# Optimization experiments

Measured on AMD Instinct MI355X. Metric: run time of the kernel, lower is better.

Reference implementation:

```python
import jax, jax.numpy as jnp
import numpy as np

N_NODES = 100000
N_EDGES = 1600000
D = 128


def setup_inputs() -> dict:
    key = jax.random.key(0)
    k1, k2, k3 = jax.random.split(key, 3)
    x = jax.random.normal(k1, (N_NODES, D), dtype=jnp.float32)
    edge_index = jax.random.randint(k2, (2, N_EDGES), 0, N_NODES, dtype=jnp.int64)
    weight = jax.random.normal(k3, (D, D), dtype=jnp.float32) * (1.0 / np.sqrt(D))
    bias = jnp.zeros((D,), dtype=jnp.float32)
    return {"x": x, "edge_index": edge_index, "weight": weight, "bias": bias}


def reference(x, edge_index, weight, bias):
    # Eval-mode forward: dropout(p=0.5, training=False) is identity.
    N = x.shape[0]
    row, col = edge_index[0], edge_index[1]  # source -> target

    # gcn_norm: add self loops (weight 1), symmetric normalization
    loop = jnp.arange(N, dtype=edge_index.dtype)
    full_row = jnp.concatenate([row, loop])
    full_col = jnp.concatenate([col, loop])
    ew = jnp.ones(full_row.shape[0], dtype=x.dtype)
    deg = jax.ops.segment_sum(ew, full_col, num_segments=N)
    deg_inv_sqrt = jnp.where(deg > 0, jax.lax.rsqrt(jnp.maximum(deg, 1e-12)), 0.0)
    norm = deg_inv_sqrt[full_row] * ew * deg_inv_sqrt[full_col]  # [E+N]

    # linear transform then gather-scale-scatter aggregation
    h = x @ weight.T  # [N, D]
    msgs = h[full_row] * norm[:, None]  # [E+N, D]
    out = jax.ops.segment_sum(msgs, full_col, num_segments=N)
    out = out + bias
    return jax.nn.relu(out)
```

## Files before the change

kernel.cpp:

```cpp
#include <hip/hip_runtime.h>

#define N_NODES 100000
#define N_EDGES 1600000
#define D 128
#define N_STRIPS (N_NODES / 32)

#define BSH   9
#define NBKT  196
#define P_BLK 160
#define EPB   (N_EDGES / P_BLK)

typedef __bf16 bf16x2 __attribute__((ext_vector_type(2)));
typedef __bf16 bf16x4 __attribute__((ext_vector_type(4)));
typedef __bf16 bf16x8 __attribute__((ext_vector_type(8)));
typedef float  f32x4  __attribute__((ext_vector_type(4)));

__global__ __launch_bounds__(256) void k_cast(const float4* __restrict__ x4,
                                              const float4* __restrict__ w4,
                                              bf16x4* __restrict__ xb4,
                                              bf16x4* __restrict__ wb4) {
    int i = blockIdx.x * 256 + threadIdx.x;
    float4 v = x4[i];
    bf16x4 o;
    o[0] = (__bf16)v.x; o[1] = (__bf16)v.y; o[2] = (__bf16)v.z; o[3] = (__bf16)v.w;
    xb4[i] = o;
    if (i < (D * D) / 4) {
        float4 u = w4[i];
        bf16x4 p;
        p[0] = (__bf16)u.x; p[1] = (__bf16)u.y; p[2] = (__bf16)u.z; p[3] = (__bf16)u.w;
        wb4[i] = p;
    }
}

__global__ __launch_bounds__(1024) void k_bhist(const int* __restrict__ col,
                                                int* __restrict__ bhist) {
    __shared__ int lh[NBKT];
    int tid = threadIdx.x, b = blockIdx.x;
    if (tid < NBKT) lh[tid] = 0;
    __syncthreads();
    int e0 = b * EPB;
    for (int e = e0 + tid; e < e0 + EPB; e += 1024)
        atomicAdd(&lh[col[e] >> BSH], 1);
    __syncthreads();
    if (tid < NBKT) bhist[tid * P_BLK + b] = lh[tid];
}

__global__ __launch_bounds__(256) void k_bscan(int* __restrict__ bhist,
                                               int* __restrict__ gtot) {
    __shared__ int buf[256];
    int k = blockIdx.x, t = threadIdx.x;
    int v = (t < P_BLK) ? bhist[k * P_BLK + t] : 0;
    buf[t] = v;
    __syncthreads();
    for (int off = 1; off < 256; off <<= 1) {
        int u = (t >= off) ? buf[t - off] : 0;
        __syncthreads();
        buf[t] += u;
        __syncthreads();
    }
    if (t < P_BLK) bhist[k * P_BLK + t] = buf[t] - v;
    if (t == 255) gtot[k] = buf[255];
}

__global__ __launch_bounds__(256) void k_gscan(const int* __restrict__ gtot,
                                               int* __restrict__ gstart) {
    __shared__ int buf[256];
    int t = threadIdx.x;
    int v = (t < NBKT) ? gtot[t] : 0;
    buf[t] = v;
    __syncthreads();
    for (int off = 1; off < 256; off <<= 1) {
        int u = (t >= off) ? buf[t - off] : 0;
        __syncthreads();
        buf[t] += u;
        __syncthreads();
    }
    if (t < NBKT) gstart[t] = buf[t] - v;
}

__global__ __launch_bounds__(1024) void k_cscatter(const int* __restrict__ row,
                                                   const int* __restrict__ col,
                                                   const int* __restrict__ bhist,
                                                   const int* __restrict__ gstart,
                                                   unsigned* __restrict__ grec) {
    __shared__ int cur[NBKT];
    int b = blockIdx.x, t = threadIdx.x;
    if (t < NBKT) cur[t] = gstart[t] + bhist[t * P_BLK + b];
    __syncthreads();
    int e0 = b * EPB;
    for (int e = e0 + t; e < e0 + EPB; e += 1024) {
        int c = col[e];
        unsigned rec = ((unsigned)row[e] << BSH) | (unsigned)(c & ((1 << BSH) - 1));
        int pos = atomicAdd(&cur[c >> BSH], 1);
        grec[pos] = rec;
    }
}

__global__ __launch_bounds__(1024) void k_fine(const unsigned* __restrict__ grec,
                                               const int* __restrict__ gtot,
                                               const int* __restrict__ gstart,
                                               int* __restrict__ deg,
                                               float* __restrict__ dis,
                                               int* __restrict__ start,
                                               int* __restrict__ srcs) {
    __shared__ int fh[512];
    __shared__ int fscan[512];
    int b = blockIdx.x;
    int tid = threadIdx.x;
    int cnt = gtot[b];
    int gs = gstart[b];
    if (tid < 512) fh[tid] = 0;
    __syncthreads();
    for (int i = tid; i < cnt; i += 1024)
        atomicAdd(&fh[grec[gs + i] & 511], 1);
    __syncthreads();
    int v = 0;
    if (tid < 512) { v = fh[tid]; fscan[tid] = v; }
    __syncthreads();
    for (int off = 1; off < 512; off <<= 1) {
        int u = 0;
        if (tid < 512 && tid >= off) u = fscan[tid - off];
        __syncthreads();
        if (tid < 512) fscan[tid] += u;
        __syncthreads();
    }
    if (tid < 512) {
        int excl = fscan[tid] - v;
        int node = (b << BSH) + tid;
        if (node < N_NODES) {
            deg[node] = v;
            dis[node] = rsqrtf((float)v + 1.0f);
            start[node] = gs + excl;
        }
        fh[tid] = excl;
    }
    __syncthreads();
    for (int i = tid; i < cnt; i += 1024) {
        unsigned r = grec[gs + i];
        int pos = atomicAdd(&fh[r & 511], 1);
        srcs[gs + pos] = (int)(r >> BSH);
    }
}

__global__ __launch_bounds__(256) void k_aggregate(const int* __restrict__ srcs,
                                                   const int* __restrict__ start,
                                                   const int* __restrict__ deg,
                                                   const __bf16* __restrict__ xb,
                                                   const float* __restrict__ dis,
                                                   float* __restrict__ out) {
    int node = (blockIdx.x * 256 + threadIdx.x) >> 6;
    int lane = threadIdx.x & 63;
    if (node >= N_NODES) return;
    int s = start[node];
    int n = deg[node];
    float dc = dis[node];
    unsigned u0 = ((const unsigned*)(xb + (size_t)node * D))[lane];
    float accx = __uint_as_float(u0 << 16) * dc * dc;
    float accy = __uint_as_float(u0 & 0xFFFF0000u) * dc * dc;

    for (int base = 0; base < n; base += 64) {
        int m = n - base; if (m > 64) m = 64;
        int   src_l = 0;
        float nr_l  = 0.f;
        if (lane < m) {
            src_l = srcs[s + base + lane];
            nr_l  = dis[src_l] * dc;
        }
        int i = 0;
        for (; i + 8 <= m; i += 8) {
            int   sv[8];
            float nv[8];
            unsigned av[8];
            #pragma unroll
            for (int j = 0; j < 8; ++j) {
                sv[j] = __shfl(src_l, i + j);
                nv[j] = __shfl(nr_l, i + j);
            }
            #pragma unroll
            for (int j = 0; j < 8; ++j)
                av[j] = ((const unsigned*)(xb + (size_t)sv[j] * D))[lane];
            #pragma unroll
            for (int j = 0; j < 8; ++j) {
                accx += __uint_as_float(av[j] << 16) * nv[j];
                accy += __uint_as_float(av[j] & 0xFFFF0000u) * nv[j];
            }
        }
        for (; i + 4 <= m; i += 4) {
            int   sv[4];
            float nv[4];
            unsigned av[4];
            #pragma unroll
            for (int j = 0; j < 4; ++j) {
                sv[j] = __shfl(src_l, i + j);
                nv[j] = __shfl(nr_l, i + j);
            }
            #pragma unroll
            for (int j = 0; j < 4; ++j)
                av[j] = ((const unsigned*)(xb + (size_t)sv[j] * D))[lane];
            #pragma unroll
            for (int j = 0; j < 4; ++j) {
                accx += __uint_as_float(av[j] << 16) * nv[j];
                accy += __uint_as_float(av[j] & 0xFFFF0000u) * nv[j];
            }
        }
        for (; i < m; ++i) {
            int   si = __shfl(src_l, i);
            float ni = __shfl(nr_l, i);
            unsigned a = ((const unsigned*)(xb + (size_t)si * D))[lane];
            accx += __uint_as_float(a << 16) * ni;
            accy += __uint_as_float(a & 0xFFFF0000u) * ni;
        }
    }
    float2 r; r.x = accx; r.y = accy;
    ((float2*)(out + (size_t)node * D))[lane] = r;
}

__global__ __launch_bounds__(256) void k_transform(const __bf16* __restrict__ wb,
                                                   const float* __restrict__ bias,
                                                   float* __restrict__ out) {
    int wave = threadIdx.x >> 6;
    int lane = threadIdx.x & 63;
    int strip = blockIdx.x * 4 + wave;
    if (strip >= N_STRIPS) return;
    int m0 = strip * 32;
    int l15 = lane & 15;
    int kq  = lane >> 4;

    bf16x8 a[2][4];
    #pragma unroll
    for (int mt = 0; mt < 2; ++mt) {
        const float* ap = out + (size_t)(m0 + mt * 16 + l15) * D + kq * 8;
        #pragma unroll
        for (int ks = 0; ks < 4; ++ks) {
            float4 lo = *(const float4*)(ap + ks * 32);
            float4 hi = *(const float4*)(ap + ks * 32 + 4);
            bf16x8 t;
            t[0] = (__bf16)lo.x; t[1] = (__bf16)lo.y;
            t[2] = (__bf16)lo.z; t[3] = (__bf16)lo.w;
            t[4] = (__bf16)hi.x; t[5] = (__bf16)hi.y;
            t[6] = (__bf16)hi.z; t[7] = (__bf16)hi.w;
            a[mt][ks] = t;
        }
    }

    f32x4 acc[2][8] = {};
    #pragma unroll
    for (int ks = 0; ks < 4; ++ks) {
        #pragma unroll
        for (int nt = 0; nt < 8; ++nt) {
            bf16x8 b = *(const bf16x8*)(wb + (size_t)(nt * 16 + l15) * D + ks * 32 + kq * 8);
            acc[0][nt] = __builtin_amdgcn_mfma_f32_16x16x32_bf16(a[0][ks], b, acc[0][nt], 0, 0, 0);
            acc[1][nt] = __builtin_amdgcn_mfma_f32_16x16x32_bf16(a[1][ks], b, acc[1][nt], 0, 0, 0);
        }
    }

    #pragma unroll
    for (int nt = 0; nt < 8; ++nt) {
        int colj = nt * 16 + l15;
        float bj = bias[colj];
        #pragma unroll
        for (int mt = 0; mt < 2; ++mt) {
            #pragma unroll
            for (int r = 0; r < 4; ++r) {
                int rowi = m0 + mt * 16 + kq * 4 + r;
                out[(size_t)rowi * D + colj] = fmaxf(acc[mt][nt][r] + bj, 0.f);
            }
        }
    }
}

extern "C" void kernel_launch(void* const* d_in, const int* in_sizes, int n_in,
                              void* d_out, int out_size, void* d_ws, size_t ws_size,
                              hipStream_t stream) {
    const float* x    = (const float*)d_in[0];
    const int*   ei   = (const int*)d_in[1];
    const float* w    = (const float*)d_in[2];
    const float* bias = (const float*)d_in[3];
    float* out = (float*)d_out;

    char* ws = (char*)d_ws;
    int*      deg    = (int*)ws;              ws += N_NODES * 4;
    float*    dis    = (float*)ws;            ws += N_NODES * 4;
    int*      start  = (int*)ws;              ws += N_NODES * 4;
    int*      bhist  = (int*)ws;              ws += NBKT * P_BLK * 4;
    int*      gtot   = (int*)ws;              ws += 256 * 4;
    int*      gstart = (int*)ws;              ws += 256 * 4;
    __bf16*   wb     = (__bf16*)ws;           ws += D * D * 2;
    unsigned* grec   = (unsigned*)ws;         ws += (size_t)N_EDGES * 4;
    int*      srcs   = (int*)ws;              ws += (size_t)N_EDGES * 4;
    __bf16*   xb     = (__bf16*)ws;

    const int* row = ei;
    const int* col = ei + N_EDGES;

    k_cast     <<<(N_NODES * D / 4) / 256, 256, 0, stream>>>(
                   (const float4*)x, (const float4*)w, (bf16x4*)xb, (bf16x4*)wb);
    k_bhist    <<<P_BLK, 1024, 0, stream>>>(col, bhist);
    k_bscan    <<<NBKT, 256, 0, stream>>>(bhist, gtot);
    k_gscan    <<<1, 256, 0, stream>>>(gtot, gstart);
    k_cscatter <<<P_BLK, 1024, 0, stream>>>(row, col, bhist, gstart, grec);
    k_fine     <<<NBKT, 1024, 0, stream>>>(grec, gtot, gstart, deg, dis, start, srcs);
    k_aggregate<<<(N_NODES * 64 + 255) / 256, 256, 0, stream>>>(srcs, start, deg, xb, dis, out);
    k_transform<<<(N_STRIPS + 3) / 4, 256, 0, stream>>>(wb, bias, out);
}
```

Measured before the change: 253.3 us.

## Fuse aggregation with MFMA transform and merge prep kernels to cut launches

Aggregation and the dense transform now share one kernel. Each block aggregates 32 nodes into shared memory and then runs the bf16 MFMA on that tile, so the intermediate fp32 output never makes a round trip through global memory. The bf16 cast and the coarse histogram are merged into one launch, and the single-block global scan is dropped by having cscatter and fine recompute the small bucket scan themselves. Launch count falls from eight to five. In exchange, each wave now handles 8 nodes serially, which lowers the parallelism available to hide gather latency, and the scan work is repeated in every block.

```diff
diff --git a/kernel.cpp b/kernel.cpp
--- a/kernel.cpp
+++ b/kernel.cpp
@@ -9,40 +9,46 @@
 #define NBKT  196
 #define P_BLK 160
 #define EPB   (N_EDGES / P_BLK)
-
-typedef __bf16 bf16x2 __attribute__((ext_vector_type(2)));
+#define CAST_BLK 256
+
 typedef __bf16 bf16x4 __attribute__((ext_vector_type(4)));
 typedef __bf16 bf16x8 __attribute__((ext_vector_type(8)));
 typedef float  f32x4  __attribute__((ext_vector_type(4)));
 
-__global__ __launch_bounds__(256) void k_cast(const float4* __restrict__ x4,
-                                              const float4* __restrict__ w4,
-                                              bf16x4* __restrict__ xb4,
-                                              bf16x4* __restrict__ wb4) {
-    int i = blockIdx.x * 256 + threadIdx.x;
-    float4 v = x4[i];
-    bf16x4 o;
-    o[0] = (__bf16)v.x; o[1] = (__bf16)v.y; o[2] = (__bf16)v.z; o[3] = (__bf16)v.w;
-    xb4[i] = o;
-    if (i < (D * D) / 4) {
-        float4 u = w4[i];
-        bf16x4 p;
-        p[0] = (__bf16)u.x; p[1] = (__bf16)u.y; p[2] = (__bf16)u.z; p[3] = (__bf16)u.w;
-        wb4[i] = p;
-    }
-}
-
-__global__ __launch_bounds__(1024) void k_bhist(const int* __restrict__ col,
-                                                int* __restrict__ bhist) {
+__global__ __launch_bounds__(1024) void k_prep(const float4* __restrict__ x4,
+                                               const float4* __restrict__ w4,
+                                               bf16x4* __restrict__ xb4,
+                                               bf16x4* __restrict__ wb4,
+                                               const int* __restrict__ col,
+                                               int* __restrict__ bhist) {
     __shared__ int lh[NBKT];
-    int tid = threadIdx.x, b = blockIdx.x;
-    if (tid < NBKT) lh[tid] = 0;
-    __syncthreads();
-    int e0 = b * EPB;
-    for (int e = e0 + tid; e < e0 + EPB; e += 1024)
-        atomicAdd(&lh[col[e] >> BSH], 1);
-    __syncthreads();
-    if (tid < NBKT) bhist[tid * P_BLK + b] = lh[tid];
+    int b = blockIdx.x, tid = threadIdx.x;
+    if (b < P_BLK) {
+        if (tid < NBKT) lh[tid] = 0;
+        __syncthreads();
+        int e0 = b * EPB;
+        for (int e = e0 + tid; e < e0 + EPB; e += 1024)
+            atomicAdd(&lh[col[e] >> BSH], 1);
+        __syncthreads();
+        if (tid < NBKT) bhist[tid * P_BLK + b] = lh[tid];
+    } else {
+        int cb = b - P_BLK;
+        const int total = N_NODES * D / 4;
+        for (int i = cb * 1024 + tid; i < total; i += CAST_BLK * 1024) {
+            float4 v = x4[i];
+            bf16x4 o;
+            o[0] = (__bf16)v.x; o[1] = (__bf16)v.y; o[2] = (__bf16)v.z; o[3] = (__bf16)v.w;
+            xb4[i] = o;
+        }
+        if (cb == 0) {
+            for (int i = tid; i < (D * D) / 4; i += 1024) {
+                float4 u = w4[i];
+                bf16x4 p;
+                p[0] = (__bf16)u.x; p[1] = (__bf16)u.y; p[2] = (__bf16)u.z; p[3] = (__bf16)u.w;
+                wb4[i] = p;
+            }
+        }
+    }
 }
 
 __global__ __launch_bounds__(256) void k_bscan(int* __restrict__ bhist,
@@ -62,30 +68,25 @@
     if (t == 255) gtot[k] = buf[255];
 }
 
-__global__ __launch_bounds__(256) void k_gscan(const int* __restrict__ gtot,
-                                               int* __restrict__ gstart) {
-    __shared__ int buf[256];
-    int t = threadIdx.x;
-    int v = (t < NBKT) ? gtot[t] : 0;
-    buf[t] = v;
-    __syncthreads();
-    for (int off = 1; off < 256; off <<= 1) {
-        int u = (t >= off) ? buf[t - off] : 0;
-        __syncthreads();
-        buf[t] += u;
-        __syncthreads();
-    }
-    if (t < NBKT) gstart[t] = buf[t] - v;
-}
-
 __global__ __launch_bounds__(1024) void k_cscatter(const int* __restrict__ row,
                                                    const int* __restrict__ col,
                                                    const int* __restrict__ bhist,
-                                                   const int* __restrict__ gstart,
+                                                   const int* __restrict__ gtot,
                                                    unsigned* __restrict__ grec) {
+    __shared__ int sbuf[256];
     __shared__ int cur[NBKT];
     int b = blockIdx.x, t = threadIdx.x;
-    if (t < NBKT) cur[t] = gstart[t] + bhist[t * P_BLK + b];
+    int v = 0;
+    if (t < 256) { v = (t < NBKT) ? gtot[t] : 0; sbuf[t] = v; }
+    __syncthreads();
+    for (int off = 1; off < 256; off <<= 1) {
+        int u = 0;
+        if (t < 256 && t >= off) u = sbuf[t - off];
+        __syncthreads();
+        if (t < 256) sbuf[t] += u;
+        __syncthreads();
+    }
+    if (t < NBKT) cur[t] = (sbuf[t] - v) + bhist[t * P_BLK + b];
     __syncthreads();
     int e0 = b * EPB;
     for (int e = e0 + t; e < e0 + EPB; e += 1024) {
@@ -98,19 +99,31 @@
 
 __global__ __launch_bounds__(1024) void k_fine(const unsigned* __restrict__ grec,
                                                const int* __restrict__ gtot,
-                                               const int* __restrict__ gstart,
                                                int* __restrict__ deg,
                                                float* __restrict__ dis,
                                                int* __restrict__ start,
                                                int* __restrict__ srcs) {
     __shared__ int fh[512];
     __shared__ int fscan[512];
+    __shared__ int sbuf[256];
+    __shared__ int gs_sh;
     int b = blockIdx.x;
     int tid = threadIdx.x;
     int cnt = gtot[b];
-    int gs = gstart[b];
+    int v0 = 0;
+    if (tid < 256) { v0 = (tid < NBKT) ? gtot[tid] : 0; sbuf[tid] = v0; }
     if (tid < 512) fh[tid] = 0;
     __syncthreads();
+    for (int off = 1; off < 256; off <<= 1) {
+        int u = 0;
+        if (tid < 256 && tid >= off) u = sbuf[tid - off];
+        __syncthreads();
+        if (tid < 256) sbuf[tid] += u;
+        __syncthreads();
+    }
+    if (tid == b) gs_sh = sbuf[tid] - v0;
+    __syncthreads();
+    int gs = gs_sh;
     for (int i = tid; i < cnt; i += 1024)
         atomicAdd(&fh[grec[gs + i] & 511], 1);
     __syncthreads();
@@ -142,104 +155,103 @@
     }
 }
 
-__global__ __launch_bounds__(256) void k_aggregate(const int* __restrict__ srcs,
-                                                   const int* __restrict__ start,
-                                                   const int* __restrict__ deg,
-                                                   const __bf16* __restrict__ xb,
-                                                   const float* __restrict__ dis,
-                                                   float* __restrict__ out) {
-    int node = (blockIdx.x * 256 + threadIdx.x) >> 6;
-    int lane = threadIdx.x & 63;
-    if (node >= N_NODES) return;
-    int s = start[node];
-    int n = deg[node];
-    float dc = dis[node];
-    unsigned u0 = ((const unsigned*)(xb + (size_t)node * D))[lane];
-    float accx = __uint_as_float(u0 << 16) * dc * dc;
-    float accy = __uint_as_float(u0 & 0xFFFF0000u) * dc * dc;
-
-    for (int base = 0; base < n; base += 64) {
-        int m = n - base; if (m > 64) m = 64;
-        int   src_l = 0;
-        float nr_l  = 0.f;
-        if (lane < m) {
-            src_l = srcs[s + base + lane];
-            nr_l  = dis[src_l] * dc;
-        }
-        int i = 0;
-        for (; i + 8 <= m; i += 8) {
-            int   sv[8];
-            float nv[8];
-            unsigned av[8];
-            #pragma unroll
-            for (int j = 0; j < 8; ++j) {
-                sv[j] = __shfl(src_l, i + j);
-                nv[j] = __shfl(nr_l, i + j);
-            }
-            #pragma unroll
-            for (int j = 0; j < 8; ++j)
-                av[j] = ((const unsigned*)(xb + (size_t)sv[j] * D))[lane];
-            #pragma unroll
-            for (int j = 0; j < 8; ++j) {
-                accx += __uint_as_float(av[j] << 16) * nv[j];
-                accy += __uint_as_float(av[j] & 0xFFFF0000u) * nv[j];
-            }
-        }
-        for (; i + 4 <= m; i += 4) {
-            int   sv[4];
-            float nv[4];
-            unsigned av[4];
-            #pragma unroll
-            for (int j = 0; j < 4; ++j) {
-                sv[j] = __shfl(src_l, i + j);
-                nv[j] = __shfl(nr_l, i + j);
-            }
-            #pragma unroll
-            for (int j = 0; j < 4; ++j)
-                av[j] = ((const unsigned*)(xb + (size_t)sv[j] * D))[lane];
-            #pragma unroll
-            for (int j = 0; j < 4; ++j) {
-                accx += __uint_as_float(av[j] << 16) * nv[j];
-                accy += __uint_as_float(av[j] & 0xFFFF0000u) * nv[j];
-            }
-        }
-        for (; i < m; ++i) {
-            int   si = __shfl(src_l, i);
-            float ni = __shfl(nr_l, i);
-            unsigned a = ((const unsigned*)(xb + (size_t)si * D))[lane];
-            accx += __uint_as_float(a << 16) * ni;
-            accy += __uint_as_float(a & 0xFFFF0000u) * ni;
-        }
-    }
-    float2 r; r.x = accx; r.y = accy;
-    ((float2*)(out + (size_t)node * D))[lane] = r;
-}
-
-__global__ __launch_bounds__(256) void k_transform(const __bf16* __restrict__ wb,
-                                                   const float* __restrict__ bias,
-                                                   float* __restrict__ out) {
-    int wave = threadIdx.x >> 6;
-    int lane = threadIdx.x & 63;
-    int strip = blockIdx.x * 4 + wave;
-    if (strip >= N_STRIPS) return;
-    int m0 = strip * 32;
+__global__ __launch_bounds__(256) void k_aggtrans(const int* __restrict__ srcs,
+                                                  const int* __restrict__ start,
+                                                  const int* __restrict__ deg,
+                                                  const __bf16* __restrict__ xb,
+                                                  const float* __restrict__ dis,
+                                                  const __bf16* __restrict__ wb,
+                                                  const float* __restrict__ bias,
+                                                  float* __restrict__ out) {
+    __shared__ float Vl[32 * 132];
+    int t = threadIdx.x;
+    int wave = t >> 6, lane = t & 63;
+    int m0 = blockIdx.x * 32;
+
+    for (int q = 0; q < 8; ++q) {
+        int nl = wave * 8 + q;
+        int node = m0 + nl;
+        int s = start[node];
+        int n = deg[node];
+        float dc = dis[node];
+        unsigned u0 = ((const unsigned*)(xb + (size_t)node * D))[lane];
+        float accx = __uint_as_float(u0 << 16) * dc * dc;
+        float accy = __uint_as_float(u0 & 0xFFFF0000u) * dc * dc;
+
+        for (int base = 0; base < n; base += 64) {
+            int m = n - base; if (m > 64) m = 64;
+            int   src_l = 0;
+            float nr_l  = 0.f;
+            if (lane < m) {
+                src_l = srcs[s + base + lane];
+                nr_l  = dis[src_l] * dc;
+            }
+            int i = 0;
+            for (; i + 8 <= m; i += 8) {
+                int   sv[8];
+                float nv[8];
+                unsigned av[8];
+                #pragma unroll
+                for (int j = 0; j < 8; ++j) {
+                    sv[j] = __shfl(src_l, i + j);
+                    nv[j] = __shfl(nr_l, i + j);
+                }
+                #pragma unroll
+                for (int j = 0; j < 8; ++j)
+                    av[j] = ((const unsigned*)(xb + (size_t)sv[j] * D))[lane];
+                #pragma unroll
+                for (int j = 0; j < 8; ++j) {
+                    accx += __uint_as_float(av[j] << 16) * nv[j];
+                    accy += __uint_as_float(av[j] & 0xFFFF0000u) * nv[j];
+                }
+            }
+            for (; i + 4 <= m; i += 4) {
+                int   sv[4];
+                float nv[4];
+                unsigned av[4];
+                #pragma unroll
+                for (int j = 0; j < 4; ++j) {
+                    sv[j] = __shfl(src_l, i + j);
+                    nv[j] = __shfl(nr_l, i + j);
+                }
+                #pragma unroll
+                for (int j = 0; j < 4; ++j)
+                    av[j] = ((const unsigned*)(xb + (size_t)sv[j] * D))[lane];
+                #pragma unroll
+                for (int j = 0; j < 4; ++j) {
+                    accx += __uint_as_float(av[j] << 16) * nv[j];
+                    accy += __uint_as_float(av[j] & 0xFFFF0000u) * nv[j];
+                }
+            }
+            for (; i < m; ++i) {
+                int   si = __shfl(src_l, i);
+                float ni = __shfl(nr_l, i);
+                unsigned a = ((const unsigned*)(xb + (size_t)si * D))[lane];
+                accx += __uint_as_float(a << 16) * ni;
+                accy += __uint_as_float(a & 0xFFFF0000u) * ni;
+            }
+        }
+        float2 r; r.x = accx; r.y = accy;
+        ((float2*)(Vl + nl * 132))[lane] = r;
+    }
+    __syncthreads();
+
     int l15 = lane & 15;
     int kq  = lane >> 4;
-
     bf16x8 a[2][4];
     #pragma unroll
     for (int mt = 0; mt < 2; ++mt) {
-        const float* ap = out + (size_t)(m0 + mt * 16 + l15) * D + kq * 8;
+        const float* ap = Vl + (mt * 16 + l15) * 132 + kq * 8;
         #pragma unroll
         for (int ks = 0; ks < 4; ++ks) {
             float4 lo = *(const float4*)(ap + ks * 32);
             float4 hi = *(const float4*)(ap + ks * 32 + 4);
-            bf16x8 t;
-            t[0] = (__bf16)lo.x; t[1] = (__bf16)lo.y;
-            t[2] = (__bf16)lo.z; t[3] = (__bf16)lo.w;
-            t[4] = (__bf16)hi.x; t[5] = (__bf16)hi.y;
-            t[6] = (__bf16)hi.z; t[7] = (__bf16)hi.w;
-            a[mt][ks] = t;
+            bf16x8 tt;
+            tt[0] = (__bf16)lo.x; tt[1] = (__bf16)lo.y;
+            tt[2] = (__bf16)lo.z; tt[3] = (__bf16)lo.w;
+            tt[4] = (__bf16)hi.x; tt[5] = (__bf16)hi.y;
+            tt[6] = (__bf16)hi.z; tt[7] = (__bf16)hi.w;
+            a[mt][ks] = tt;
         }
     }
 
@@ -284,7 +296,6 @@
     int*      start  = (int*)ws;              ws += N_NODES * 4;
     int*      bhist  = (int*)ws;              ws += NBKT * P_BLK * 4;
     int*      gtot   = (int*)ws;              ws += 256 * 4;
-    int*      gstart = (int*)ws;              ws += 256 * 4;
     __bf16*   wb     = (__bf16*)ws;           ws += D * D * 2;
     unsigned* grec   = (unsigned*)ws;         ws += (size_t)N_EDGES * 4;
     int*      srcs   = (int*)ws;              ws += (size_t)N_EDGES * 4;
@@ -293,13 +304,11 @@
     const int* row = ei;
     const int* col = ei + N_EDGES;
 
-    k_cast     <<<(N_NODES * D / 4) / 256, 256, 0, stream>>>(
-                   (const float4*)x, (const float4*)w, (bf16x4*)xb, (bf16x4*)wb);
-    k_bhist    <<<P_BLK, 1024, 0, stream>>>(col, bhist);
-    k_bscan    <<<NBKT, 256, 0, stream>>>(bhist, gtot);
-    k_gscan    <<<1, 256, 0, stream>>>(gtot, gstart);
-    k_cscatter <<<P_BLK, 1024, 0, stream>>>(row, col, bhist, gstart, grec);
-    k_fine     <<<NBKT, 1024, 0, stream>>>(grec, gtot, gstart, deg, dis, start, srcs);
-    k_aggregate<<<(N_NODES * 64 + 255) / 256, 256, 0, stream>>>(srcs, start, deg, xb, dis, out);
-    k_transform<<<(N_STRIPS + 3) / 4, 256, 0, stream>>>(wb, bias, out);
-}
+    k_prep    <<<P_BLK + CAST_BLK, 1024, 0, stream>>>(
+                  (const float4*)x, (const float4*)w, (bf16x4*)xb, (bf16x4*)wb,
+                  col, bhist);
+    k_bscan   <<<NBKT, 256, 0, stream>>>(bhist, gtot);
+    k_cscatter<<<P_BLK, 1024, 0, stream>>>(row, col, bhist, gtot, grec);
+    k_fine    <<<NBKT, 1024, 0, stream>>>(grec, gtot, deg, dis, start, srcs);
+    k_aggtrans<<<N_STRIPS, 256, 0, stream>>>(srcs, start, deg, xb, dis, wb, bias, out);
+}
```

New measurement: 320.6 us. +26.6%, slower.
